# Kernel optimization log

Measured on AMD Instinct MI355X. Metric: run time of the kernel, lower is better.

## Reference

```python
import jax, jax.numpy as jnp
import numpy as np

N, E, IN, HID, H, G, OUT = 50000, 800000, 128, 96, 8, 64, 10
D = HID // H  # per-head dim = 12


def setup_inputs() -> dict:
    key = jax.random.key(0)
    ks = jax.random.split(key, 24)
    s = 0.1
    inp = {
        'x': jax.random.normal(ks[0], (N, IN), jnp.float32),
        'src': jax.random.randint(ks[1], (E,), 0, N, jnp.int32),
        'dst': jax.random.randint(ks[2], (E,), 0, N, jnp.int32),
        'graph_id': jax.random.randint(ks[3], (N,), 0, G, jnp.int32),
        # GraphConv layers (norm='both', weight + bias)
        'W1': jax.random.normal(ks[4], (IN, HID), jnp.float32) * s,
        'b1': jnp.zeros((HID,), jnp.float32),
        'W2': jax.random.normal(ks[5], (HID, HID), jnp.float32) * s,
        'b2': jnp.zeros((HID,), jnp.float32),
        # 3 GATv2 layers, stacked params
        'Ws': jax.random.normal(ks[6], (3, HID, HID), jnp.float32) * s,
        'bs': jnp.zeros((3, HID), jnp.float32),
        'Wd': jax.random.normal(ks[7], (3, HID, HID), jnp.float32) * s,
        'bd': jnp.zeros((3, HID), jnp.float32),
        'attn': jax.random.normal(ks[8], (3, H, D), jnp.float32) * s,
        # classifier MLP (dropout is identity at inference)
        'Wc1': jax.random.normal(ks[9], (HID, HID), jnp.float32) * s,
        'bc1': jnp.zeros((HID,), jnp.float32),
        'Wc2': jax.random.normal(ks[10], (HID, HID // 2), jnp.float32) * s,
        'bc2': jnp.zeros((HID // 2,), jnp.float32),
        'Wc3': jax.random.normal(ks[11], (HID // 2, OUT), jnp.float32) * s,
        'bc3': jnp.zeros((OUT,), jnp.float32),
    }
    return inp


def _graph_conv(h, W, b, src, dst):
    # DGL GraphConv, norm='both', allow_zero_in_degree (degrees clamped to >=1)
    ones = jnp.ones((E,), h.dtype)
    deg_out = jnp.clip(jax.ops.segment_sum(ones, src, N), 1.0)
    deg_in = jnp.clip(jax.ops.segment_sum(ones, dst, N), 1.0)
    h = (h * (deg_out ** -0.5)[:, None]) @ W          # [N, out]
    agg = jax.ops.segment_sum(h[src], dst, N)          # sum over in-edges
    return agg * (deg_in ** -0.5)[:, None] + b


def _gatv2(h, Ws, bs, Wd, bd, attn, src, dst):
    fs = (h @ Ws + bs).reshape(N, H, D)
    fd = (h @ Wd + bd).reshape(N, H, D)
    e = jax.nn.leaky_relu(fs[src] + fd[dst], 0.2)      # [E, H, D]
    logits = jnp.einsum('ehd,hd->eh', e, attn)         # [E, H]
    # edge softmax over incoming edges of each dst node
    m = jax.ops.segment_max(logits, dst, N)            # [N, H]
    ex = jnp.exp(logits - m[dst])
    den = jax.ops.segment_sum(ex, dst, N)              # [N, H]
    a = ex / den[dst]                                  # [E, H]
    rst = jax.ops.segment_sum(a[:, :, None] * fs[src], dst, N)  # [N, H, D]
    return jax.nn.relu(rst).reshape(N, HID)            # activation=relu, then view


def reference(x, src, dst, graph_id, W1, b1, W2, b2, Ws, bs, Wd, bd, attn,
              Wc1, bc1, Wc2, bc2, Wc3, bc3):
    h = jax.nn.relu(_graph_conv(x, W1, b1, src, dst))
    h = jax.nn.relu(_graph_conv(h, W2, b2, src, dst))
    for i in range(3):
        h = _gatv2(h, Ws[i], bs[i], Wd[i], bd[i], attn[i], src, dst)
    # dgl.max_nodes: per-graph max readout
    hg = jax.ops.segment_max(h, graph_id, G)           # [G, HID]
    z = jax.nn.relu(hg @ Wc1 + bc1)
    z = jax.nn.relu(z @ Wc2 + bc2)
    return z @ Wc3 + bc3                               # [G, OUT]
```

## Files before the change

### kernel.cpp

```cpp
#include <hip/hip_runtime.h>
#include <hip/hip_bf16.h>

#define Nn 50000
#define Ee 800000
#define INF_ 128
#define HIDF 96
#define HH 8
#define DD 12
#define GG 64
#define OUTF 10

#define SCAN_CHUNK 512
#define SCAN_BLOCKS ((Nn + SCAN_CHUNK - 1) / SCAN_CHUNK)
#define RB 128

#define HCHK 256
#define HCHKE (Ee / HCHK)
#define NW 12512
#define DBIN 64

__global__ __launch_bounds__(256) void hist_lds(const int* __restrict__ src,
                                                const int* __restrict__ dst,
                                                unsigned int* __restrict__ partS,
                                                unsigned int* __restrict__ partD) {
    __shared__ unsigned int h[NW];
    int b = blockIdx.x, t = threadIdx.x;
    for (int i = t; i < NW; i += 256) h[i] = 0u;
    __syncthreads();
    int base = b * HCHKE;
    for (int i = t; i < HCHKE; i += 256) {
        int d = dst[base + i];
        atomicAdd(&h[d >> 2], 1u << ((d & 3) * 8));
    }
    __syncthreads();
    for (int i = t; i < NW; i += 256) { partD[(size_t)b * NW + i] = h[i]; h[i] = 0u; }
    __syncthreads();
    for (int i = t; i < HCHKE; i += 256) {
        int s = src[base + i];
        atomicAdd(&h[s >> 2], 1u << ((s & 3) * 8));
    }
    __syncthreads();
    for (int i = t; i < NW; i += 256) partS[(size_t)b * NW + i] = h[i];
}

__global__ void hist_reduce(const unsigned int* __restrict__ partS,
                            const unsigned int* __restrict__ partD,
                            int* __restrict__ cnt_in, int* __restrict__ cnt_out) {
    int w = blockIdx.x * 256 + threadIdx.x;
    if (w >= NW) return;
    unsigned int totS = 0u, totD = 0u;
    for (int b = 0; b < HCHK; ++b) {
        totS += partS[(size_t)b * NW + w];
        totD += partD[(size_t)b * NW + w];
    }
#pragma unroll
    for (int j = 0; j < 4; ++j) {
        int k = w * 4 + j;
        if (k < Nn) {
            cnt_in[k]  = (int)((totD >> (j * 8)) & 0xFFu);
            cnt_out[k] = (int)((totS >> (j * 8)) & 0xFFu);
        }
    }
}

__global__ __launch_bounds__(256) void scan1_kernel(const int* __restrict__ cnt_in,
                                                    int* __restrict__ row_start,
                                                    int* __restrict__ blk_sum, int N) {
    __shared__ int part[256];
    int t = threadIdx.x;
    int base = blockIdx.x * SCAN_CHUNK;
    int i0 = base + 2 * t, i1 = i0 + 1;
    int a = (i0 < N) ? cnt_in[i0] : 0;
    int b = (i1 < N) ? cnt_in[i1] : 0;
    int s = a + b;
    part[t] = s;
    __syncthreads();
    for (int off = 1; off < 256; off <<= 1) {
        int v = (t >= off) ? part[t - off] : 0;
        __syncthreads();
        part[t] += v;
        __syncthreads();
    }
    int excl = part[t] - s;
    if (i0 < N) row_start[i0] = excl;
    if (i1 < N) row_start[i1] = excl + a;
    if (t == 255) blk_sum[blockIdx.x] = part[255];
}

__global__ __launch_bounds__(128) void scan2_kernel(const int* __restrict__ blk_sum,
                                                    int* __restrict__ blk_off,
                                                    int* __restrict__ row_start, int N) {
    __shared__ int part[128];
    int t = threadIdx.x;
    int v0 = (t < SCAN_BLOCKS) ? blk_sum[t] : 0;
    part[t] = v0;
    __syncthreads();
    for (int off = 1; off < 128; off <<= 1) {
        int v = (t >= off) ? part[t - off] : 0;
        __syncthreads();
        part[t] += v;
        __syncthreads();
    }
    blk_off[t] = part[t] - v0;
    if (t == 127) row_start[N] = part[127];
}

__global__ __launch_bounds__(256) void scan3_kernel(int* __restrict__ row_start,
                                                    const int* __restrict__ blk_off, int N) {
    int t = threadIdx.x;
    int base = blockIdx.x * SCAN_CHUNK;
    int off = blk_off[blockIdx.x];
    int i0 = base + 2 * t, i1 = i0 + 1;
    if (i0 < N) row_start[i0] += off;
    if (i1 < N) row_start[i1] += off;
}

__global__ void node_setup(const int* __restrict__ cnt_in, const int* __restrict__ cnt_out,
                           const int* __restrict__ row_start, int* __restrict__ cursor,
                           float* __restrict__ degI_is, float* __restrict__ degO_is, int N) {
    int n = blockIdx.x * 256 + threadIdx.x;
    if (n < N) {
        cursor[n] = row_start[n];
        degI_is[n] = rsqrtf((float)max(cnt_in[n], 1));
        degO_is[n] = rsqrtf((float)max(cnt_out[n], 1));
    }
}

__global__ void fill_kernel(const int* __restrict__ src, const int* __restrict__ dst,
                            int* __restrict__ cursor, int* __restrict__ csr_src, int E) {
    int e = blockIdx.x * 256 + threadIdx.x;
    if (e < E) {
        int slot = atomicAdd(&cursor[dst[e]], 1);
        csr_src[slot] = src[e];
    }
}

__global__ __launch_bounds__(256) void deg_hist(const int* __restrict__ cnt_in,
                                                int* __restrict__ dcnt, int N) {
    __shared__ int h[DBIN];
    int t = threadIdx.x;
    if (t < DBIN) h[t] = 0;
    __syncthreads();
    int n = blockIdx.x * 256 + t;
    if (n < N) atomicAdd(&h[min(cnt_in[n], DBIN - 1)], 1);
    __syncthreads();
    if (t < DBIN && h[t]) atomicAdd(&dcnt[t], h[t]);
}

__global__ __launch_bounds__(64) void deg_scan(const int* __restrict__ dcnt,
                                               int* __restrict__ dcur) {
    __shared__ int p[DBIN];
    int t = threadIdx.x;
    int v0 = dcnt[t];
    p[t] = v0;
    __syncthreads();
    for (int o = 1; o < DBIN; o <<= 1) {
        int v = (t >= o) ? p[t - o] : 0;
        __syncthreads();
        p[t] += v;
        __syncthreads();
    }
    dcur[t] = p[t] - v0;
}

__global__ __launch_bounds__(256) void perm_fill(const int* __restrict__ cnt_in,
                                                 int* __restrict__ dcur,
                                                 int* __restrict__ perm, int N) {
    __shared__ int lh[DBIN];
    __shared__ int lbase[DBIN];
    int t = threadIdx.x;
    if (t < DBIN) lh[t] = 0;
    __syncthreads();
    int n = blockIdx.x * 256 + t;
    int bin = 0, lslot = 0;
    if (n < N) {
        bin = min(cnt_in[n], DBIN - 1);
        lslot = atomicAdd(&lh[bin], 1);
    }
    __syncthreads();
    if (t < DBIN) lbase[t] = lh[t] ? atomicAdd(&dcur[t], lh[t]) : 0;
    __syncthreads();
    if (n < N) perm[lbase[bin] + lslot] = n;
}

__global__ __launch_bounds__(192) void gemm96(const float* __restrict__ A, int K,
                                              const float* __restrict__ W,
                                              const float* __restrict__ bias,
                                              const float* __restrict__ rowScale,
                                              float* __restrict__ out, int N) {
    __shared__ float A_lds[64 * 36];
    __shared__ float W_lds[32 * 96];
    const int t = threadIdx.x;
    const int row0 = blockIdx.x * 64;
    const int tcol = t % 24;
    const int trow = t / 24;
    float acc[8][4];
#pragma unroll
    for (int i = 0; i < 8; ++i)
#pragma unroll
        for (int j = 0; j < 4; ++j) acc[i][j] = 0.f;

    for (int k0 = 0; k0 < K; k0 += 32) {
        for (int i = t; i < 32 * 24; i += 192) {
            ((float4*)W_lds)[i] = ((const float4*)W)[(size_t)k0 * 24 + i];
        }
        for (int i = t; i < 64 * 8; i += 192) {
            int r = i / 8, kk = i % 8;
            int gr = row0 + r;
            float4 v = make_float4(0.f, 0.f, 0.f, 0.f);
            if (gr < N) {
                v = *((const float4*)(A + (size_t)gr * K + k0 + kk * 4));
                if (rowScale) {
                    float s = rowScale[gr];
                    v.x *= s; v.y *= s; v.z *= s; v.w *= s;
                }
            }
            *((float4*)(A_lds + r * 36 + kk * 4)) = v;
        }
        __syncthreads();
#pragma unroll
        for (int kk4 = 0; kk4 < 8; ++kk4) {
            float4 a[8];
#pragma unroll
            for (int i = 0; i < 8; ++i)
                a[i] = *((const float4*)(A_lds + (trow + 8 * i) * 36 + kk4 * 4));
#pragma unroll
            for (int kk = 0; kk < 4; ++kk) {
                float4 wv = *((const float4*)(W_lds + (kk4 * 4 + kk) * 96 + tcol * 4));
#pragma unroll
                for (int i = 0; i < 8; ++i) {
                    float av = (kk == 0) ? a[i].x : (kk == 1) ? a[i].y : (kk == 2) ? a[i].z : a[i].w;
                    acc[i][0] = fmaf(av, wv.x, acc[i][0]);
                    acc[i][1] = fmaf(av, wv.y, acc[i][1]);
                    acc[i][2] = fmaf(av, wv.z, acc[i][2]);
                    acc[i][3] = fmaf(av, wv.w, acc[i][3]);
                }
            }
        }
        __syncthreads();
    }
    float4 b4 = bias ? *((const float4*)(bias + tcol * 4)) : make_float4(0.f, 0.f, 0.f, 0.f);
#pragma unroll
    for (int i = 0; i < 8; ++i) {
        int gr = row0 + trow + 8 * i;
        if (gr < N) {
            float4 o = make_float4(acc[i][0] + b4.x, acc[i][1] + b4.y,
                                   acc[i][2] + b4.z, acc[i][3] + b4.w);
            *((float4*)(out + (size_t)gr * 96 + tcol * 4)) = o;
        }
    }
}

__global__ __launch_bounds__(192) void gemm96x2(const float* __restrict__ A,
                                                const float* __restrict__ W1_, const float* __restrict__ b1_,
                                                const float* __restrict__ W2_, const float* __restrict__ b2_,
                                                float* __restrict__ out1, float* __restrict__ out2, int N) {
    __shared__ float A_lds[64 * 36];
    __shared__ float W_lds[2 * 32 * 96];
    const int t = threadIdx.x;
    const int row0 = blockIdx.x * 64;
    const int tcol = t % 24;
    const int trow = t / 24;
    float acc1[8][4], acc2[8][4];
#pragma unroll
    for (int i = 0; i < 8; ++i)
#pragma unroll
        for (int j = 0; j < 4; ++j) { acc1[i][j] = 0.f; acc2[i][j] = 0.f; }

    for (int k0 = 0; k0 < 96; k0 += 32) {
        for (int i = t; i < 32 * 24; i += 192) {
            ((float4*)W_lds)[i] = ((const float4*)W1_)[(size_t)k0 * 24 + i];
            ((float4*)(W_lds + 32 * 96))[i] = ((const float4*)W2_)[(size_t)k0 * 24 + i];
        }
        for (int i = t; i < 64 * 8; i += 192) {
            int r = i / 8, kk = i % 8;
            int gr = row0 + r;
            float4 v = make_float4(0.f, 0.f, 0.f, 0.f);
            if (gr < N) v = *((const float4*)(A + (size_t)gr * 96 + k0 + kk * 4));
            *((float4*)(A_lds + r * 36 + kk * 4)) = v;
        }
        __syncthreads();
#pragma unroll
        for (int kk4 = 0; kk4 < 8; ++kk4) {
            float4 a[8];
#pragma unroll
            for (int i = 0; i < 8; ++i)
                a[i] = *((const float4*)(A_lds + (trow + 8 * i) * 36 + kk4 * 4));
#pragma unroll
            for (int kk = 0; kk < 4; ++kk) {
                float4 wv1 = *((const float4*)(W_lds + (kk4 * 4 + kk) * 96 + tcol * 4));
                float4 wv2 = *((const float4*)(W_lds + 32 * 96 + (kk4 * 4 + kk) * 96 + tcol * 4));
#pragma unroll
                for (int i = 0; i < 8; ++i) {
                    float av = (kk == 0) ? a[i].x : (kk == 1) ? a[i].y : (kk == 2) ? a[i].z : a[i].w;
                    acc1[i][0] = fmaf(av, wv1.x, acc1[i][0]);
                    acc1[i][1] = fmaf(av, wv1.y, acc1[i][1]);
                    acc1[i][2] = fmaf(av, wv1.z, acc1[i][2]);
                    acc1[i][3] = fmaf(av, wv1.w, acc1[i][3]);
                    acc2[i][0] = fmaf(av, wv2.x, acc2[i][0]);
                    acc2[i][1] = fmaf(av, wv2.y, acc2[i][1]);
                    acc2[i][2] = fmaf(av, wv2.z, acc2[i][2]);
                    acc2[i][3] = fmaf(av, wv2.w, acc2[i][3]);
                }
            }
        }
        __syncthreads();
    }
    float4 bb1 = *((const float4*)(b1_ + tcol * 4));
    float4 bb2 = *((const float4*)(b2_ + tcol * 4));
#pragma unroll
    for (int i = 0; i < 8; ++i) {
        int gr = row0 + trow + 8 * i;
        if (gr < N) {
            float4 o1 = make_float4(acc1[i][0] + bb1.x, acc1[i][1] + bb1.y,
                                    acc1[i][2] + bb1.z, acc1[i][3] + bb1.w);
            float4 o2 = make_float4(acc2[i][0] + bb2.x, acc2[i][1] + bb2.y,
                                    acc2[i][2] + bb2.z, acc2[i][3] + bb2.w);
            *((float4*)(out1 + (size_t)gr * 96 + tcol * 4)) = o1;
            *((float4*)(out2 + (size_t)gr * 96 + tcol * 4)) = o2;
        }
    }
}

__global__ __launch_bounds__(192) void gc_agg(const float* __restrict__ hW,
                                              const int* __restrict__ row_start,
                                              const int* __restrict__ csr_src,
                                              const float* __restrict__ degI_is,
                                              const float* __restrict__ bias,
                                              const int* __restrict__ perm,
                                              float* __restrict__ hout, int N) {
    int tid = blockIdx.x * 192 + threadIdx.x;
    int p = tid / 24;
    int c = (tid % 24) * 4;
    if (p >= N) return;
    int n = perm[p];
    int beg = row_start[n], end = row_start[n + 1];
    float4 s = make_float4(0.f, 0.f, 0.f, 0.f);
    int e = beg;
    for (; e + 4 <= end; e += 4) {
        int i0 = csr_src[e], i1 = csr_src[e + 1], i2 = csr_src[e + 2], i3 = csr_src[e + 3];
        float4 v0 = *(const float4*)(hW + (size_t)i0 * 96 + c);
        float4 v1 = *(const float4*)(hW + (size_t)i1 * 96 + c);
        float4 v2 = *(const float4*)(hW + (size_t)i2 * 96 + c);
        float4 v3 = *(const float4*)(hW + (size_t)i3 * 96 + c);
        s.x += (v0.x + v1.x) + (v2.x + v3.x);
        s.y += (v0.y + v1.y) + (v2.y + v3.y);
        s.z += (v0.z + v1.z) + (v2.z + v3.z);
        s.w += (v0.w + v1.w) + (v2.w + v3.w);
    }
    for (; e < end; ++e) {
        int i0 = csr_src[e];
        float4 v0 = *(const float4*)(hW + (size_t)i0 * 96 + c);
        s.x += v0.x; s.y += v0.y; s.z += v0.z; s.w += v0.w;
    }
    float dn = degI_is[n];
    float4 b = *(const float4*)(bias + c);
    float4 o;
    o.x = fmaxf(fmaf(s.x, dn, b.x), 0.f);
    o.y = fmaxf(fmaf(s.y, dn, b.y), 0.f);
    o.z = fmaxf(fmaf(s.z, dn, b.z), 0.f);
    o.w = fmaxf(fmaf(s.w, dn, b.w), 0.f);
    *(float4*)(hout + (size_t)n * 96 + c) = o;
}

__global__ __launch_bounds__(256) void gat_agg(const float* __restrict__ fs,
                                               const float* __restrict__ fd,
                                               const float* __restrict__ attn,
                                               const int* __restrict__ row_start,
                                               const int* __restrict__ csr_src,
                                               const int* __restrict__ perm,
                                               float* __restrict__ hout, int N) {
    int tid = blockIdx.x * 256 + threadIdx.x;
    int p = tid >> 3, hd = tid & 7;
    if (p >= N) return;
    int n = perm[p];
    float att[12], fdv[12];
    {
        const float4* ap = (const float4*)(attn + hd * 12);
        float4 a0 = ap[0], a1 = ap[1], a2 = ap[2];
        att[0]=a0.x; att[1]=a0.y; att[2]=a0.z; att[3]=a0.w;
        att[4]=a1.x; att[5]=a1.y; att[6]=a1.z; att[7]=a1.w;
        att[8]=a2.x; att[9]=a2.y; att[10]=a2.z; att[11]=a2.w;
        const float4* dp = (const float4*)(fd + (size_t)n * 96 + hd * 12);
        float4 d0 = dp[0], d1 = dp[1], d2 = dp[2];
        fdv[0]=d0.x; fdv[1]=d0.y; fdv[2]=d0.z; fdv[3]=d0.w;
        fdv[4]=d1.x; fdv[5]=d1.y; fdv[6]=d1.z; fdv[7]=d1.w;
        fdv[8]=d2.x; fdv[9]=d2.y; fdv[10]=d2.z; fdv[11]=d2.w;
    }
    int beg = row_start[n], end = row_start[n + 1];
    float m = -3.0e38f, den = 0.f;
    float acc[12];
#pragma unroll
    for (int d = 0; d < 12; ++d) acc[d] = 0.f;

    auto process = [&](const float4& s0, const float4& s1, const float4& s2) {
        float fsv[12];
        fsv[0]=s0.x; fsv[1]=s0.y; fsv[2]=s0.z; fsv[3]=s0.w;
        fsv[4]=s1.x; fsv[5]=s1.y; fsv[6]=s1.z; fsv[7]=s1.w;
        fsv[8]=s2.x; fsv[9]=s2.y; fsv[10]=s2.z; fsv[11]=s2.w;
        float logit = 0.f;
#pragma unroll
        for (int d = 0; d < 12; ++d) {
            float u = fsv[d] + fdv[d];
            u = u > 0.f ? u : 0.2f * u;
            logit = fmaf(u, att[d], logit);
        }
        float nm = fmaxf(m, logit);
        float cc = __expf(m - nm);
        float w  = __expf(logit - nm);
        den = fmaf(den, cc, w);
#pragma unroll
        for (int d = 0; d < 12; ++d) acc[d] = fmaf(acc[d], cc, w * fsv[d]);
        m = nm;
    };

    int e = beg;
    for (; e + 4 <= end; e += 4) {
        int i0 = csr_src[e], i1 = csr_src[e + 1], i2 = csr_src[e + 2], i3 = csr_src[e + 3];
        const float4* p0 = (const float4*)(fs + (size_t)i0 * 96 + hd * 12);
        const float4* p1 = (const float4*)(fs + (size_t)i1 * 96 + hd * 12);
        const float4* p2 = (const float4*)(fs + (size_t)i2 * 96 + hd * 12);
        const float4* p3 = (const float4*)(fs + (size_t)i3 * 96 + hd * 12);
        float4 a0 = p0[0], a1 = p0[1], a2 = p0[2];
        float4 b0 = p1[0], b1 = p1[1], b2 = p1[2];
        float4 c0 = p2[0], c1 = p2[1], c2 = p2[2];
        float4 d0 = p3[0], d1 = p3[1], d2 = p3[2];
        process(a0, a1, a2);
        process(b0, b1, b2);
        process(c0, c1, c2);
        process(d0, d1, d2);
    }
    for (; e < end; ++e) {
        int i0 = csr_src[e];
        const float4* p0 = (const float4*)(fs + (size_t)i0 * 96 + hd * 12);
        float4 a0 = p0[0], a1 = p0[1], a2 = p0[2];
        process(a0, a1, a2);
    }
    float inv = den > 0.f ? 1.f / den : 0.f;
    float* op = hout + (size_t)n * 96 + hd * 12;
#pragma unroll
    for (int d = 0; d < 12; ++d) op[d] = fmaxf(acc[d] * inv, 0.f);
}

__global__ __launch_bounds__(384) void readout_partial(const float* __restrict__ h,
                                                       const int* __restrict__ graph_id,
                                                       float* __restrict__ partial, int N) {
    __shared__ int lhg[GG * 96];
    int t = threadIdx.x;
    for (int i = t; i < GG * 96; i += 384) lhg[i] = 0;
    __syncthreads();
    int f = t % 96, nl = t / 96;
    for (int n0 = blockIdx.x * 4; n0 < N; n0 += RB * 4) {
        int n = n0 + nl;
        if (n < N) {
            int g = graph_id[n];
            float v = h[(size_t)n * 96 + f];
            atomicMax(&lhg[g * 96 + f], __float_as_int(v));
        }
    }
    __syncthreads();
    for (int i = t; i < GG * 96; i += 384)
        partial[(size_t)blockIdx.x * (GG * 96) + i] = __int_as_float(lhg[i]);
}

__global__ void readout_reduce(const float* __restrict__ partial, float* __restrict__ hg) {
    int i = blockIdx.x * 256 + threadIdx.x;
    if (i < GG * 96) {
        float m = 0.f;
        for (int b = 0; b < RB; ++b) m = fmaxf(m, partial[(size_t)b * (GG * 96) + i]);
        hg[i] = m;
    }
}

__global__ __launch_bounds__(96) void mlp_kernel(const float* __restrict__ hg,
                                                 const float* __restrict__ Wc1, const float* __restrict__ bc1,
                                                 const float* __restrict__ Wc2, const float* __restrict__ bc2,
                                                 const float* __restrict__ Wc3, const float* __restrict__ bc3,
                                                 float* __restrict__ out) {
    int g = blockIdx.x;
    int t = threadIdx.x;
    __shared__ float z0[96], z1[96], z2[48];
    z0[t] = hg[(size_t)g * 96 + t];
    __syncthreads();
    float s = bc1[t];
    for (int k = 0; k < 96; ++k) s = fmaf(z0[k], Wc1[k * 96 + t], s);
    z1[t] = fmaxf(s, 0.f);
    __syncthreads();
    if (t < 48) {
        float s2 = bc2[t];
        for (int k = 0; k < 96; ++k) s2 = fmaf(z1[k], Wc2[k * 48 + t], s2);
        z2[t] = fmaxf(s2, 0.f);
    }
    __syncthreads();
    if (t < 10) {
        float s3 = bc3[t];
        for (int k = 0; k < 48; ++k) s3 = fmaf(z2[k], Wc3[k * 10 + t], s3);
        out[(size_t)g * 10 + t] = s3;
    }
}

extern "C" void kernel_launch(void* const* d_in, const int* in_sizes, int n_in,
                              void* d_out, int out_size, void* d_ws, size_t ws_size,
                              hipStream_t stream) {
    const float* x        = (const float*)d_in[0];
    const int*   src      = (const int*)d_in[1];
    const int*   dst      = (const int*)d_in[2];
    const int*   graph_id = (const int*)d_in[3];
    const float* W1  = (const float*)d_in[4];
    const float* b1  = (const float*)d_in[5];
    const float* W2  = (const float*)d_in[6];
    const float* b2  = (const float*)d_in[7];
    const float* Ws  = (const float*)d_in[8];
    const float* bs  = (const float*)d_in[9];
    const float* Wd  = (const float*)d_in[10];
    const float* bd  = (const float*)d_in[11];
    const float* attn = (const float*)d_in[12];
    const float* Wc1 = (const float*)d_in[13];
    const float* bc1 = (const float*)d_in[14];
    const float* Wc2 = (const float*)d_in[15];
    const float* bc2 = (const float*)d_in[16];
    const float* Wc3 = (const float*)d_in[17];
    const float* bc3 = (const float*)d_in[18];
    float* out = (float*)d_out;

    char* ws = (char*)d_ws;
    size_t off = 0;
    auto alloc = [&](size_t bytes) {
        char* p = ws + off;
        off = (off + bytes + 255) & ~(size_t)255;
        return p;
    };
    int*   cnt_in    = (int*)alloc(Nn * 4);
    int*   cnt_out   = (int*)alloc(Nn * 4);
    int*   row_start = (int*)alloc((Nn + 1) * 4);
    int*   cursor    = (int*)alloc(Nn * 4);
    int*   csr_src   = (int*)alloc(Ee * 4);
    int*   perm      = (int*)alloc(Nn * 4);
    float* degI_is   = (float*)alloc(Nn * 4);
    float* degO_is   = (float*)alloc(Nn * 4);
    float* bufH      = (float*)alloc((size_t)Nn * 96 * 4);
    float* bufT      = (float*)alloc((size_t)Nn * 96 * 4);
    float* bufFd     = (float*)alloc((size_t)Nn * 96 * 4);
    float* hg        = (float*)alloc(GG * 96 * 4);
    float* partial   = (float*)alloc((size_t)RB * GG * 96 * 4);
    int*   blk_sum   = (int*)alloc(128 * 4);
    int*   blk_off   = (int*)alloc(128 * 4);
    int*   dcnt      = (int*)alloc(DBIN * 4);
    int*   dcur      = (int*)alloc(DBIN * 4);

    unsigned int* partS = (unsigned int*)bufT;
    unsigned int* partD = (unsigned int*)bufFd;

    hipMemsetAsync(dcnt, 0, DBIN * 4, stream);

    hist_lds<<<HCHK, 256, 0, stream>>>(src, dst, partS, partD);
    hist_reduce<<<(NW + 255) / 256, 256, 0, stream>>>(partS, partD, cnt_in, cnt_out);
    scan1_kernel<<<SCAN_BLOCKS, 256, 0, stream>>>(cnt_in, row_start, blk_sum, Nn);
    scan2_kernel<<<1, 128, 0, stream>>>(blk_sum, blk_off, row_start, Nn);
    scan3_kernel<<<SCAN_BLOCKS, 256, 0, stream>>>(row_start, blk_off, Nn);
    node_setup<<<(Nn + 255) / 256, 256, 0, stream>>>(cnt_in, cnt_out, row_start, cursor,
                                                     degI_is, degO_is, Nn);
    fill_kernel<<<(Ee + 255) / 256, 256, 0, stream>>>(src, dst, cursor, csr_src, Ee);

    deg_hist<<<(Nn + 255) / 256, 256, 0, stream>>>(cnt_in, dcnt, Nn);
    deg_scan<<<1, 64, 0, stream>>>(dcnt, dcur);
    perm_fill<<<(Nn + 255) / 256, 256, 0, stream>>>(cnt_in, dcur, perm, Nn);

    int gemm_blocks = (Nn + 63) / 64;
    int agg_blocks  = (Nn * 24 + 191) / 192;
    int gat_blocks  = (Nn * 8 + 255) / 256;

    gemm96<<<gemm_blocks, 192, 0, stream>>>(x, 128, W1, nullptr, degO_is, bufT, Nn);
    gc_agg<<<agg_blocks, 192, 0, stream>>>(bufT, row_start, csr_src, degI_is, b1, perm, bufH, Nn);
    gemm96<<<gemm_blocks, 192, 0, stream>>>(bufH, 96, W2, nullptr, degO_is, bufT, Nn);
    gc_agg<<<agg_blocks, 192, 0, stream>>>(bufT, row_start, csr_src, degI_is, b2, perm, bufH, Nn);

    for (int l = 0; l < 3; ++l) {
        const float* Wsl = Ws + (size_t)l * 96 * 96;
        const float* bsl = bs + (size_t)l * 96;
        const float* Wdl = Wd + (size_t)l * 96 * 96;
        const float* bdl = bd + (size_t)l * 96;
        const float* atl = attn + (size_t)l * 96;
        gemm96x2<<<gemm_blocks, 192, 0, stream>>>(bufH, Wsl, bsl, Wdl, bdl, bufT, bufFd, Nn);
        gat_agg<<<gat_blocks, 256, 0, stream>>>(bufT, bufFd, atl, row_start, csr_src, perm, bufH, Nn);
    }

    readout_partial<<<RB, 384, 0, stream>>>(bufH, graph_id, partial, Nn);
    readout_reduce<<<(GG * 96 + 255) / 256, 256, 0, stream>>>(partial, hg);
    mlp_kernel<<<GG, 96, 0, stream>>>(hg, Wc1, bc1, Wc2, bc2, Wc3, bc3, out);
}
```

Before: 676.4 us.

## Build CSR deterministically from LDS histogram slots; reorder nodes by descending degree; dual softmax accumulators

The histogram kernel now records each edge's local slot from the LDS atomic's return value, and the reduce kernel becomes an exclusive scan over per-block partial counts. The fill kernel then places edges without global atomics on a cursor array, and the cursor initialisation is dropped. The degree-bucket permutation is reversed so high in-degree nodes are scheduled first, which is meant to reduce tail imbalance. The GAT aggregation keeps two independent online-softmax accumulators merged at the end, which shortens the dependency chain in the unrolled loop at the cost of more registers and an extra edge_slot buffer.

```diff
diff --git a/kernel.cpp b/kernel.cpp
--- a/kernel.cpp
+++ b/kernel.cpp
@@ -22,7 +22,8 @@
 __global__ __launch_bounds__(256) void hist_lds(const int* __restrict__ src,
                                                 const int* __restrict__ dst,
                                                 unsigned int* __restrict__ partS,
-                                                unsigned int* __restrict__ partD) {
+                                                unsigned int* __restrict__ partD,
+                                                int* __restrict__ edge_slot) {
     __shared__ unsigned int h[NW];
     int b = blockIdx.x, t = threadIdx.x;
     for (int i = t; i < NW; i += 256) h[i] = 0u;
@@ -30,7 +31,8 @@
     int base = b * HCHKE;
     for (int i = t; i < HCHKE; i += 256) {
         int d = dst[base + i];
-        atomicAdd(&h[d >> 2], 1u << ((d & 3) * 8));
+        unsigned int old = atomicAdd(&h[d >> 2], 1u << ((d & 3) * 8));
+        edge_slot[base + i] = (int)((old >> ((d & 3) * 8)) & 0xFFu);
     }
     __syncthreads();
     for (int i = t; i < NW; i += 256) { partD[(size_t)b * NW + i] = h[i]; h[i] = 0u; }
@@ -43,21 +45,24 @@
     for (int i = t; i < NW; i += 256) partS[(size_t)b * NW + i] = h[i];
 }
 
-__global__ void hist_reduce(const unsigned int* __restrict__ partS,
-                            const unsigned int* __restrict__ partD,
-                            int* __restrict__ cnt_in, int* __restrict__ cnt_out) {
+__global__ void hist_scan(unsigned int* __restrict__ partD,
+                          const unsigned int* __restrict__ partS,
+                          int* __restrict__ cnt_in, int* __restrict__ cnt_out) {
     int w = blockIdx.x * 256 + threadIdx.x;
     if (w >= NW) return;
-    unsigned int totS = 0u, totD = 0u;
+    unsigned int run = 0u, totS = 0u;
     for (int b = 0; b < HCHK; ++b) {
-        totS += partS[(size_t)b * NW + w];
-        totD += partD[(size_t)b * NW + w];
+        size_t idx = (size_t)b * NW + w;
+        unsigned int v = partD[idx];
+        partD[idx] = run;
+        run += v;
+        totS += partS[idx];
     }
 #pragma unroll
     for (int j = 0; j < 4; ++j) {
         int k = w * 4 + j;
         if (k < Nn) {
-            cnt_in[k]  = (int)((totD >> (j * 8)) & 0xFFu);
+            cnt_in[k]  = (int)((run >> (j * 8)) & 0xFFu);
             cnt_out[k] = (int)((totS >> (j * 8)) & 0xFFu);
         }
     }
@@ -116,22 +121,28 @@
 }
 
 __global__ void node_setup(const int* __restrict__ cnt_in, const int* __restrict__ cnt_out,
-                           const int* __restrict__ row_start, int* __restrict__ cursor,
                            float* __restrict__ degI_is, float* __restrict__ degO_is, int N) {
     int n = blockIdx.x * 256 + threadIdx.x;
     if (n < N) {
-        cursor[n] = row_start[n];
         degI_is[n] = rsqrtf((float)max(cnt_in[n], 1));
         degO_is[n] = rsqrtf((float)max(cnt_out[n], 1));
     }
 }
 
-__global__ void fill_kernel(const int* __restrict__ src, const int* __restrict__ dst,
-                            int* __restrict__ cursor, int* __restrict__ csr_src, int E) {
-    int e = blockIdx.x * 256 + threadIdx.x;
-    if (e < E) {
-        int slot = atomicAdd(&cursor[dst[e]], 1);
-        csr_src[slot] = src[e];
+__global__ __launch_bounds__(256) void fill_kernel(const int* __restrict__ src,
+                                                   const int* __restrict__ dst,
+                                                   const int* __restrict__ row_start,
+                                                   const unsigned int* __restrict__ partD,
+                                                   const int* __restrict__ edge_slot,
+                                                   int* __restrict__ csr_src) {
+    int b = blockIdx.x, t = threadIdx.x;
+    int base = b * HCHKE;
+    size_t po = (size_t)b * NW;
+    for (int i = t; i < HCHKE; i += 256) {
+        int e = base + i;
+        int d = dst[e];
+        int cb = (int)((partD[po + (d >> 2)] >> ((d & 3) * 8)) & 0xFFu);
+        csr_src[row_start[d] + cb + edge_slot[e]] = src[e];
     }
 }
 
@@ -142,7 +153,7 @@
     if (t < DBIN) h[t] = 0;
     __syncthreads();
     int n = blockIdx.x * 256 + t;
-    if (n < N) atomicAdd(&h[min(cnt_in[n], DBIN - 1)], 1);
+    if (n < N) atomicAdd(&h[DBIN - 1 - min(cnt_in[n], DBIN - 1)], 1);
     __syncthreads();
     if (t < DBIN && h[t]) atomicAdd(&dcnt[t], h[t]);
 }
@@ -174,7 +185,7 @@
     int n = blockIdx.x * 256 + t;
     int bin = 0, lslot = 0;
     if (n < N) {
-        bin = min(cnt_in[n], DBIN - 1);
+        bin = DBIN - 1 - min(cnt_in[n], DBIN - 1);
         lslot = atomicAdd(&lh[bin], 1);
     }
     __syncthreads();
@@ -388,12 +399,13 @@
         fdv[8]=d2.x; fdv[9]=d2.y; fdv[10]=d2.z; fdv[11]=d2.w;
     }
     int beg = row_start[n], end = row_start[n + 1];
-    float m = -3.0e38f, den = 0.f;
-    float acc[12];
-#pragma unroll
-    for (int d = 0; d < 12; ++d) acc[d] = 0.f;
-
-    auto process = [&](const float4& s0, const float4& s1, const float4& s2) {
+    float m0 = -3.0e38f, den0 = 0.f, m1 = -3.0e38f, den1 = 0.f;
+    float A0[12], A1[12];
+#pragma unroll
+    for (int d = 0; d < 12; ++d) { A0[d] = 0.f; A1[d] = 0.f; }
+
+    auto proc = [&](const float4& s0, const float4& s1, const float4& s2,
+                    float& m, float& den, float* acc) {
         float fsv[12];
         fsv[0]=s0.x; fsv[1]=s0.y; fsv[2]=s0.z; fsv[3]=s0.w;
         fsv[4]=s1.x; fsv[5]=s1.y; fsv[6]=s1.z; fsv[7]=s1.w;
@@ -425,21 +437,25 @@
         float4 b0 = p1[0], b1 = p1[1], b2 = p1[2];
         float4 c0 = p2[0], c1 = p2[1], c2 = p2[2];
         float4 d0 = p3[0], d1 = p3[1], d2 = p3[2];
-        process(a0, a1, a2);
-        process(b0, b1, b2);
-        process(c0, c1, c2);
-        process(d0, d1, d2);
+        proc(a0, a1, a2, m0, den0, A0);
+        proc(b0, b1, b2, m1, den1, A1);
+        proc(c0, c1, c2, m0, den0, A0);
+        proc(d0, d1, d2, m1, den1, A1);
     }
     for (; e < end; ++e) {
         int i0 = csr_src[e];
         const float4* p0 = (const float4*)(fs + (size_t)i0 * 96 + hd * 12);
         float4 a0 = p0[0], a1 = p0[1], a2 = p0[2];
-        process(a0, a1, a2);
-    }
+        proc(a0, a1, a2, m0, den0, A0);
+    }
+    float nm = fmaxf(m0, m1);
+    float c0 = __expf(m0 - nm), c1 = __expf(m1 - nm);
+    float den = den0 * c0 + den1 * c1;
     float inv = den > 0.f ? 1.f / den : 0.f;
     float* op = hout + (size_t)n * 96 + hd * 12;
 #pragma unroll
-    for (int d = 0; d < 12; ++d) op[d] = fmaxf(acc[d] * inv, 0.f);
+    for (int d = 0; d < 12; ++d)
+        op[d] = fmaxf((A0[d] * c0 + A1[d] * c1) * inv, 0.f);
 }
 
 __global__ __launch_bounds__(384) void readout_partial(const float* __restrict__ h,
@@ -533,7 +549,7 @@
     int*   cnt_in    = (int*)alloc(Nn * 4);
     int*   cnt_out   = (int*)alloc(Nn * 4);
     int*   row_start = (int*)alloc((Nn + 1) * 4);
-    int*   cursor    = (int*)alloc(Nn * 4);
+    int*   edge_slot = (int*)alloc(Ee * 4);
     int*   csr_src   = (int*)alloc(Ee * 4);
     int*   perm      = (int*)alloc(Nn * 4);
     float* degI_is   = (float*)alloc(Nn * 4);
@@ -553,14 +569,13 @@
 
     hipMemsetAsync(dcnt, 0, DBIN * 4, stream);
 
-    hist_lds<<<HCHK, 256, 0, stream>>>(src, dst, partS, partD);
-    hist_reduce<<<(NW + 255) / 256, 256, 0, stream>>>(partS, partD, cnt_in, cnt_out);
+    hist_lds<<<HCHK, 256, 0, stream>>>(src, dst, partS, partD, edge_slot);
+    hist_scan<<<(NW + 255) / 256, 256, 0, stream>>>(partD, partS, cnt_in, cnt_out);
     scan1_kernel<<<SCAN_BLOCKS, 256, 0, stream>>>(cnt_in, row_start, blk_sum, Nn);
     scan2_kernel<<<1, 128, 0, stream>>>(blk_sum, blk_off, row_start, Nn);
     scan3_kernel<<<SCAN_BLOCKS, 256, 0, stream>>>(row_start, blk_off, Nn);
-    node_setup<<<(Nn + 255) / 256, 256, 0, stream>>>(cnt_in, cnt_out, row_start, cursor,
-                                                     degI_is, degO_is, Nn);
-    fill_kernel<<<(Ee + 255) / 256, 256, 0, stream>>>(src, dst, cursor, csr_src, Ee);
+    node_setup<<<(Nn + 255) / 256, 256, 0, stream>>>(cnt_in, cnt_out, degI_is, degO_is, Nn);
+    fill_kernel<<<HCHK, 256, 0, stream>>>(src, dst, row_start, partD, edge_slot, csr_src);
 
     deg_hist<<<(Nn + 255) / 256, 256, 0, stream>>>(cnt_in, dcnt, Nn);
     deg_scan<<<1, 64, 0, stream>>>(dcnt, dcur);
```

New measurement: 648.4 us. 4.1% less time.
